# Optimization experiments

Measured on AMD Instinct MI355X. Metric: run time of the kernel, lower is better.

The kernel has to match this reference:

```python
import jax, jax.numpy as jnp
import numpy as np

B, T, D, L, H = 8, 2048, 128, 4, 2
HD = D // H
NITEMS = 200000
EPS = 1e-8  # RMSNorm eps and HSTU denom eps


def _rms(x, s):
    return x * jax.lax.rsqrt(jnp.mean(x * x, axis=-1, keepdims=True) + EPS) * s


def setup_inputs() -> dict:
    key = jax.random.key(0)
    ks = jax.random.split(key, 16)
    g = lambda k, shape: jax.random.normal(k, shape, jnp.float32) * 0.02
    inp = {}
    inp["log_seqs"] = jax.random.randint(ks[0], (B, T), 1, NITEMS + 1)
    inp["attn_mask"] = jnp.tril(jnp.ones((T, T), dtype=bool))  # causal keep-mask
    inp["item_table"] = g(ks[1], (NITEMS + 1, D))
    inp["pos_table"] = g(ks[2], (2 * T + 1, D))
    inp["emb_ln_s"] = jnp.ones((D,), jnp.float32)
    inp["ln1_s"] = jnp.ones((L, D), jnp.float32)
    inp["Uw"] = g(ks[3], (L, D, D)); inp["Ub"] = jnp.zeros((L, D), jnp.float32)
    inp["Vw"] = g(ks[4], (L, D, D)); inp["Vb"] = jnp.zeros((L, D), jnp.float32)
    inp["Qw"] = g(ks[5], (L, D, D)); inp["Qb"] = jnp.zeros((L, D), jnp.float32)
    inp["Kw"] = g(ks[6], (L, D, D)); inp["Kb"] = jnp.zeros((L, D), jnp.float32)
    inp["f2w"] = g(ks[7], (L, D, D)); inp["f2b"] = jnp.zeros((L, D), jnp.float32)
    inp["hstu_ln_s"] = jnp.ones((L, D), jnp.float32)
    inp["ln2_s"] = jnp.ones((L, D), jnp.float32)
    inp["c1w"] = g(ks[8], (L, D, D)); inp["c1b"] = jnp.zeros((L, D), jnp.float32)
    inp["c2w"] = g(ks[9], (L, D, D)); inp["c2b"] = jnp.zeros((L, D), jnp.float32)
    inp["last_ln_s"] = jnp.ones((D,), jnp.float32)
    return inp


def reference(log_seqs, attn_mask, item_table, pos_table, emb_ln_s, ln1_s,
              Uw, Ub, Vw, Vb, Qw, Qb, Kw, Kb, f2w, f2b, hstu_ln_s, ln2_s,
              c1w, c1b, c2w, c2b, last_ln_s):
    positions = jnp.arange(1, T + 1)
    x = item_table[log_seqs] + pos_table[positions][None]  # (B,T,D)
    x = _rms(x, emb_ln_s)
    keep = attn_mask[None, None]  # (1,1,T,T) broadcast over (B,H,T,T)
    scale = 1.0 / np.sqrt(HD)
    for i in range(L):
        q = _rms(x, ln1_s[i])  # pre-norm (norm_first)
        U = jax.nn.silu(q @ Uw[i] + Ub[i])
        V = jax.nn.silu(q @ Vw[i] + Vb[i])
        Q = jax.nn.silu(q @ Qw[i] + Qb[i])
        K = jax.nn.silu(q @ Kw[i] + Kb[i])
        Qh = Q.reshape(B, T, H, HD)
        Kh = K.reshape(B, T, H, HD)
        Vh = V.reshape(B, T, H, HD)
        logits = jnp.einsum('bthd,bshd->bhts', Qh, Kh) * scale  # (B,H,T,T)
        A = jnp.maximum(jax.nn.silu(logits), 0.0)  # SiLU then clamp_min(0)
        A = jnp.where(keep, A, 0.0)
        denom = jnp.sum(A, axis=-1, keepdims=True)
        A = jnp.where(denom > 1e-12, A / (denom + EPS), 0.0)
        AV = jnp.einsum('bhts,bshd->bthd', A, Vh).reshape(B, T, D)
        y = (_rms(AV, hstu_ln_s[i]) * U) @ f2w[i] + f2b[i]
        x = x + y
        f = _rms(x, ln2_s[i])  # pre-norm for FFN
        h = jax.nn.gelu(f @ c1w[i] + c1b[i], approximate=False)  # Conv1d k=1 == Linear
        x = x + (h @ c2w[i] + c2b[i])
    return _rms(x, last_ln_s)
```

## Files before the change

kernel.cpp:

```cpp
#include <hip/hip_runtime.h>
#include <hip/hip_bf16.h>

typedef __bf16 bf16x8 __attribute__((ext_vector_type(8)));
typedef float f32x4 __attribute__((ext_vector_type(4)));
using bf16 = __hip_bfloat16;

constexpr int T = 2048;
constexpr int M = 8 * 2048;

__device__ inline float ldf(const void* p, size_t i, int isf32) {
  if (isf32) return ((const float*)p)[i];
  unsigned u = ((const unsigned short*)p)[i];
  return __uint_as_float(u << 16);
}
__device__ inline float bf2f(unsigned short u) { return __uint_as_float((unsigned)u << 16); }
__device__ inline unsigned short bfb(float x) {
  __hip_bfloat16 h = __float2bfloat16(x);
  return *reinterpret_cast<unsigned short*>(&h);
}

struct PPtrs { const void* p[12]; };

__global__ void detect_convert_k(const void* __restrict__ item, PPtrs ps,
                                 float* __restrict__ params, int* __restrict__ flagp) {
  __shared__ int cnt[4];
  __shared__ int flagLDS;
  int tid = threadIdx.x;
  unsigned short lo = ((const unsigned short*)item)[tid * 2];
  float a = fabsf(bf2f(lo));
  bool okb = (a > 1e-5f) && (a < 0.5f);
  unsigned long long m = __ballot(okb);
  if ((tid & 63) == 0) cnt[tid >> 6] = __popcll(m);
  __syncthreads();
  if (tid == 0) {
    int tot = cnt[0] + cnt[1] + cnt[2] + cnt[3];
    int f = (tot < 128) ? 1 : 0;
    flagLDS = f; *flagp = f;
  }
  __syncthreads();
  int f = flagLDS;
  const int lens[12] = {128, 512, 512, 512, 128, 512, 512, 512, 512, 512, 512, 512};
  int off = 0;
  for (int j = 0; j < 12; ++j) {
    for (int i = tid; i < lens[j]; i += 256) params[off + i] = ldf(ps.p[j], i, f);
    off += lens[j];
  }
}

struct WPtrs { const void* p[7]; };

__global__ void transpose_w_k(WPtrs w, bf16* __restrict__ dst, const int* __restrict__ flagp) {
  int f = *flagp;
  int l = blockIdx.x, wi = blockIdx.y;
  const void* s = w.p[wi];
  size_t sbase = (size_t)l * 16384;
  bf16* d = dst + ((size_t)wi * 4 + l) * 16384;
  for (int i = 0; i < 64; ++i) {
    int e = i * 256 + threadIdx.x;
    d[e] = __float2bfloat16(ldf(s, sbase + (size_t)(e & 127) * 128 + (e >> 7), f));
  }
}

__device__ inline void issueW(const bf16* wt, bf16x8 (&w)[4][8], int quad, int l16) {
  #pragma unroll
  for (int kk = 0; kk < 4; ++kk)
    #pragma unroll
    for (int nt = 0; nt < 8; ++nt)
      w[kk][nt] = *(const bf16x8*)(wt + (size_t)(nt * 16 + l16) * 128 + kk * 32 + quad * 8);
}
__device__ inline void mfma_stage(const bf16x8 (&a)[4], const bf16x8 (&w)[4][8], f32x4 (&acc)[8]) {
  #pragma unroll
  for (int kk = 0; kk < 4; ++kk)
    #pragma unroll
    for (int nt = 0; nt < 8; ++nt)
      acc[nt] = __builtin_amdgcn_mfma_f32_16x16x32_bf16(a[kk], w[kk][nt], acc[nt], 0, 0, 0);
}
__device__ inline void zero8(f32x4 (&acc)[8]) {
  #pragma unroll
  for (int i = 0; i < 8; ++i) acc[i] = (f32x4){0.f, 0.f, 0.f, 0.f};
}
__device__ inline void readA(const bf16* aw, bf16x8 (&a)[4], int quad, int l16) {
  #pragma unroll
  for (int kk = 0; kk < 4; ++kk)
    a[kk] = *(const bf16x8*)&aw[l16 * 136 + kk * 32 + quad * 8];
}
__device__ inline void buildA_rms(const float (&xr)[8][4], const float* scale, bf16* aw,
                                  int quad, int l16) {
  float s8[8];
  #pragma unroll
  for (int nt = 0; nt < 8; ++nt) s8[nt] = scale[nt * 16 + l16];
  #pragma unroll
  for (int r = 0; r < 4; ++r) {
    float ss = 0.f;
    #pragma unroll
    for (int nt = 0; nt < 8; ++nt) ss += xr[nt][r] * xr[nt][r];
    ss += __shfl_xor(ss, 1); ss += __shfl_xor(ss, 2);
    ss += __shfl_xor(ss, 4); ss += __shfl_xor(ss, 8);
    float rs = rsqrtf(ss * (1.f / 128.f) + 1e-8f);
    #pragma unroll
    for (int nt = 0; nt < 8; ++nt)
      aw[(quad * 4 + r) * 136 + nt * 16 + l16] = __float2bfloat16(xr[nt][r] * rs * s8[nt]);
  }
}
__device__ inline void epi_silu_store(const f32x4 (&acc)[8], const float* bias, bf16* outg,
                                      int row0, int quad, int l16, float mulf) {
  #pragma unroll
  for (int nt = 0; nt < 8; ++nt) {
    int col = nt * 16 + l16; float bv = bias[col];
    #pragma unroll
    for (int r = 0; r < 4; ++r) {
      float v = acc[nt][r] + bv;
      v = v / (1.f + __expf(-v)) * mulf;
      outg[(size_t)(row0 + quad * 4 + r) * 128 + col] = __float2bfloat16(v);
    }
  }
}
__device__ inline void epi_silu_vt(const f32x4 (&acc)[8], const float* bias, bf16* vtg,
                                   int row0, int quad, int l16) {
  #pragma unroll
  for (int nt = 0; nt < 8; ++nt) {
    int col = nt * 16 + l16; float bv = bias[col];
    int h = col >> 6, hd = col & 63;
    #pragma unroll
    for (int r = 0; r < 4; ++r) {
      int gr = row0 + quad * 4 + r; int b = gr >> 11, t = gr & 2047;
      float v = acc[nt][r] + bv; v = v / (1.f + __expf(-v));
      vtg[((size_t)(b * 2 + h) * 64 + hd) * 2048 + t] = __float2bfloat16(v);
    }
  }
}
__device__ inline void epi_addx(const f32x4 (&acc)[8], const float* bias, float (&xr)[8][4],
                                int l16) {
  #pragma unroll
  for (int nt = 0; nt < 8; ++nt) {
    float bv = bias[nt * 16 + l16];
    #pragma unroll
    for (int r = 0; r < 4; ++r) xr[nt][r] += acc[nt][r] + bv;
  }
}

__device__ inline void qkvu_stages(const float (&xr)[8][4], bf16* aw, const bf16* wT,
    const float* params, int lnext, bf16* Ug, bf16* Qg, bf16* Kg, bf16* VTg,
    int row0, int quad, int l16) {
  buildA_rms(xr, params + 128 + lnext * 128, aw, quad, l16);
  bf16x8 a[4]; readA(aw, a, quad, l16);
  bf16x8 w[4][8]; f32x4 acc[8];
  const float* pb = params + 1792;
  issueW(wT + (size_t)(0 * 4 + lnext) * 16384, w, quad, l16);
  zero8(acc); mfma_stage(a, w, acc);
  issueW(wT + (size_t)(1 * 4 + lnext) * 16384, w, quad, l16);
  epi_silu_store(acc, pb + 0 * 512 + lnext * 128, Ug, row0, quad, l16, 1.f);
  zero8(acc); mfma_stage(a, w, acc);
  issueW(wT + (size_t)(2 * 4 + lnext) * 16384, w, quad, l16);
  epi_silu_vt(acc, pb + 1 * 512 + lnext * 128, VTg, row0, quad, l16);
  zero8(acc); mfma_stage(a, w, acc);
  issueW(wT + (size_t)(3 * 4 + lnext) * 16384, w, quad, l16);
  epi_silu_store(acc, pb + 2 * 512 + lnext * 128, Qg, row0, quad, l16, 0.125f);
  zero8(acc); mfma_stage(a, w, acc);
  epi_silu_store(acc, pb + 3 * 512 + lnext * 128, Kg, row0, quad, l16, 1.f);
}

__global__ __launch_bounds__(256) void pre_k(const int* __restrict__ seqs,
    const void* __restrict__ item, const void* __restrict__ pos, const bf16* __restrict__ wT,
    const float* __restrict__ params, float* __restrict__ xg, bf16* __restrict__ Ug,
    bf16* __restrict__ Qg, bf16* __restrict__ Kg, bf16* __restrict__ VTg,
    const int* __restrict__ flagp) {
  __shared__ __align__(16) bf16 awAll[4][16 * 136 + 8];
  int f = *flagp;
  int tid = threadIdx.x, wv = tid >> 6, lane = tid & 63, quad = lane >> 4, l16 = lane & 15;
  bf16* aw = awAll[wv];
  int row0 = blockIdx.x * 64 + wv * 16;
  int idxs[4];
  #pragma unroll
  for (int r = 0; r < 4; ++r) idxs[r] = seqs[row0 + quad * 4 + r];
  float xr[8][4];
  #pragma unroll
  for (int nt = 0; nt < 8; ++nt) {
    int col = nt * 16 + l16;
    #pragma unroll
    for (int r = 0; r < 4; ++r) {
      int gr = row0 + quad * 4 + r; int t = gr & 2047;
      xr[nt][r] = ldf(item, (size_t)idxs[r] * 128 + col, f)
                + ldf(pos, (size_t)(t + 1) * 128 + col, f);
    }
  }
  {
    float s8[8];
    #pragma unroll
    for (int nt = 0; nt < 8; ++nt) s8[nt] = params[nt * 16 + l16];
    #pragma unroll
    for (int r = 0; r < 4; ++r) {
      float ss = 0.f;
      #pragma unroll
      for (int nt = 0; nt < 8; ++nt) ss += xr[nt][r] * xr[nt][r];
      ss += __shfl_xor(ss, 1); ss += __shfl_xor(ss, 2);
      ss += __shfl_xor(ss, 4); ss += __shfl_xor(ss, 8);
      float rs = rsqrtf(ss * (1.f / 128.f) + 1e-8f);
      #pragma unroll
      for (int nt = 0; nt < 8; ++nt) xr[nt][r] *= rs * s8[nt];
    }
  }
  #pragma unroll
  for (int nt = 0; nt < 8; ++nt)
    #pragma unroll
    for (int r = 0; r < 4; ++r)
      xg[(size_t)(row0 + quad * 4 + r) * 128 + nt * 16 + l16] = xr[nt][r];
  qkvu_stages(xr, aw, wT, params, 0, Ug, Qg, Kg, VTg, row0, quad, l16);
}

__global__ __launch_bounds__(256) void post_k(int l, float* __restrict__ xg,
    const float* __restrict__ avg, bf16* __restrict__ Ug, bf16* __restrict__ Qg,
    bf16* __restrict__ Kg, bf16* __restrict__ VTg, const bf16* __restrict__ wT,
    const float* __restrict__ params, void* __restrict__ dout, const int* __restrict__ flagp) {
  __shared__ __align__(16) bf16 awAll[4][16 * 136 + 8];
  int tid = threadIdx.x, wv = tid >> 6, lane = tid & 63, quad = lane >> 4, l16 = lane & 15;
  bf16* aw = awAll[wv];
  int row0 = blockIdx.x * 64 + wv * 16;
  bf16x8 w[4][8]; f32x4 acc[8];
  issueW(wT + (size_t)(16 + l) * 16384, w, quad, l16);
  float xr[8][4], av[8][4], uu[8][4];
  #pragma unroll
  for (int nt = 0; nt < 8; ++nt) {
    int col = nt * 16 + l16;
    #pragma unroll
    for (int r = 0; r < 4; ++r) {
      size_t off = (size_t)(row0 + quad * 4 + r) * 128 + col;
      xr[nt][r] = xg[off];
      av[nt][r] = avg[off];
      uu[nt][r] = bf2f(((const unsigned short*)Ug)[off]);
    }
  }
  {
    const float* hs = params + 640 + l * 128;
    float s8[8];
    #pragma unroll
    for (int nt = 0; nt < 8; ++nt) s8[nt] = hs[nt * 16 + l16];
    #pragma unroll
    for (int r = 0; r < 4; ++r) {
      float ss = 0.f;
      #pragma unroll
      for (int nt = 0; nt < 8; ++nt) ss += av[nt][r] * av[nt][r];
      ss += __shfl_xor(ss, 1); ss += __shfl_xor(ss, 2);
      ss += __shfl_xor(ss, 4); ss += __shfl_xor(ss, 8);
      float rs = rsqrtf(ss * (1.f / 128.f) + 1e-8f);
      #pragma unroll
      for (int nt = 0; nt < 8; ++nt)
        aw[(quad * 4 + r) * 136 + nt * 16 + l16] =
            __float2bfloat16(av[nt][r] * rs * s8[nt] * uu[nt][r]);
    }
  }
  bf16x8 a[4]; readA(aw, a, quad, l16);
  zero8(acc); mfma_stage(a, w, acc);
  issueW(wT + (size_t)(20 + l) * 16384, w, quad, l16);
  epi_addx(acc, params + 3840 + l * 128, xr, l16);
  buildA_rms(xr, params + 1152 + l * 128, aw, quad, l16);
  readA(aw, a, quad, l16);
  zero8(acc); mfma_stage(a, w, acc);
  issueW(wT + (size_t)(24 + l) * 16384, w, quad, l16);
  {
    const float* bb = params + 4352 + l * 128;
    #pragma unroll
    for (int nt = 0; nt < 8; ++nt) {
      int col = nt * 16 + l16; float bv = bb[col];
      #pragma unroll
      for (int r = 0; r < 4; ++r) {
        float v = acc[nt][r] + bv;
        v = 0.5f * v * (1.f + erff(v * 0.70710678118f));
        aw[(quad * 4 + r) * 136 + col] = __float2bfloat16(v);
      }
    }
  }
  readA(aw, a, quad, l16);
  zero8(acc); mfma_stage(a, w, acc);
  epi_addx(acc, params + 4864 + l * 128, xr, l16);
  if (l == 3) {
    int f = *flagp;
    const float* ls = params + 1664;
    float s8[8];
    #pragma unroll
    for (int nt = 0; nt < 8; ++nt) s8[nt] = ls[nt * 16 + l16];
    #pragma unroll
    for (int r = 0; r < 4; ++r) {
      float ss = 0.f;
      #pragma unroll
      for (int nt = 0; nt < 8; ++nt) ss += xr[nt][r] * xr[nt][r];
      ss += __shfl_xor(ss, 1); ss += __shfl_xor(ss, 2);
      ss += __shfl_xor(ss, 4); ss += __shfl_xor(ss, 8);
      float rs = rsqrtf(ss * (1.f / 128.f) + 1e-8f);
      #pragma unroll
      for (int nt = 0; nt < 8; ++nt) {
        size_t off = (size_t)(row0 + quad * 4 + r) * 128 + nt * 16 + l16;
        float o = xr[nt][r] * rs * s8[nt];
        if (f) ((float*)dout)[off] = o; else ((unsigned short*)dout)[off] = bfb(o);
      }
    }
    return;
  }
  #pragma unroll
  for (int nt = 0; nt < 8; ++nt)
    #pragma unroll
    for (int r = 0; r < 4; ++r)
      xg[(size_t)(row0 + quad * 4 + r) * 128 + nt * 16 + l16] = xr[nt][r];
  qkvu_stages(xr, aw, wT, params, l + 1, Ug, Qg, Kg, VTg, row0, quad, l16);
}

__device__ inline void fk_loadK(const bf16* kbase, bf16x8 (&kf)[2][4], int quad, int l16) {
  #pragma unroll
  for (int kk = 0; kk < 2; ++kk)
    #pragma unroll
    for (int nt = 0; nt < 4; ++nt)
      kf[kk][nt] = *(const bf16x8*)(kbase + (size_t)(nt * 16 + l16) * 128 + kk * 32 + quad * 8);
}

__device__ inline void flash_body(int kt, int ntile, const bf16* kga, const bf16* vba,
    const bf16x8 (&qf)[2][2], const bf16x8 (&kc)[2][4], bf16x8 (&kn)[2][4],
    f32x4 (&oacc)[2][4], f32x4 (&dacc)[2], const bf16x8& onesf,
    bf16* sm, int r0, int quad, int l16) {
  int s0 = kt * 64;
  bf16x8 vf[2][4];
  #pragma unroll
  for (int kk = 0; kk < 2; ++kk)
    #pragma unroll
    for (int nt = 0; nt < 4; ++nt)
      vf[kk][nt] = *(const bf16x8*)(vba + (size_t)(nt * 16 + l16) * 2048 + s0 + kk * 32 + quad * 8);
  f32x4 sacc[2][4] = {};
  #pragma unroll
  for (int kk = 0; kk < 2; ++kk)
    #pragma unroll
    for (int nt = 0; nt < 4; ++nt) {
      sacc[0][nt] = __builtin_amdgcn_mfma_f32_16x16x32_bf16(qf[0][kk], kc[kk][nt], sacc[0][nt], 0, 0, 0);
      sacc[1][nt] = __builtin_amdgcn_mfma_f32_16x16x32_bf16(qf[1][kk], kc[kk][nt], sacc[1][nt], 0, 0, 0);
    }
  if (kt + 2 < ntile) fk_loadK(kga + (size_t)(s0 + 128) * 128, kn, quad, l16);
  #pragma unroll
  for (int mi = 0; mi < 2; ++mi) {
    int trow = r0 + mi * 16 + quad * 4;
    #pragma unroll
    for (int nt = 0; nt < 4; ++nt) {
      int sc = s0 + nt * 16 + l16;
      #pragma unroll
      for (int r = 0; r < 4; ++r) {
        float v = sacc[mi][nt][r];
        float aa = (sc <= trow + r && v > 0.f) ? v / (1.f + __expf(-v)) : 0.f;
        sm[(mi * 16 + quad * 4 + r) * 72 + nt * 16 + l16] = __float2bfloat16(aa);
      }
    }
  }
  #pragma unroll
  for (int kk = 0; kk < 2; ++kk) {
    bf16x8 af0 = *(const bf16x8*)&sm[l16 * 72 + kk * 32 + quad * 8];
    bf16x8 af1 = *(const bf16x8*)&sm[(16 + l16) * 72 + kk * 32 + quad * 8];
    #pragma unroll
    for (int nt = 0; nt < 4; ++nt) {
      oacc[0][nt] = __builtin_amdgcn_mfma_f32_16x16x32_bf16(af0, vf[kk][nt], oacc[0][nt], 0, 0, 0);
      oacc[1][nt] = __builtin_amdgcn_mfma_f32_16x16x32_bf16(af1, vf[kk][nt], oacc[1][nt], 0, 0, 0);
    }
    dacc[0] = __builtin_amdgcn_mfma_f32_16x16x32_bf16(af0, onesf, dacc[0], 0, 0, 0);
    dacc[1] = __builtin_amdgcn_mfma_f32_16x16x32_bf16(af1, onesf, dacc[1], 0, 0, 0);
  }
}

__global__ __launch_bounds__(128, 2) void flash_k(const bf16* __restrict__ Qg,
    const bf16* __restrict__ Kg, const bf16* __restrict__ VTg, float* __restrict__ avg) {
  __shared__ __align__(16) bf16 smem[2 * 2304];
  int q32 = 63 - (int)blockIdx.x;
  int bh = blockIdx.y, b = bh >> 1, h = bh & 1;
  int tid = threadIdx.x, p = tid >> 6, lane = tid & 63, quad = lane >> 4, l16 = lane & 15;
  int r0 = q32 * 32;
  bf16* sm = smem + p * 2304;
  const bf16* kga = Kg + (size_t)b * 2048 * 128 + h * 64;
  const bf16* vba = VTg + (size_t)bh * 64 * 2048;
  const bf16* qbase = Qg + ((size_t)b * 2048 + r0) * 128 + h * 64;
  bf16x8 qf[2][2];
  #pragma unroll
  for (int mi = 0; mi < 2; ++mi)
    #pragma unroll
    for (int kk = 0; kk < 2; ++kk)
      qf[mi][kk] = *(const bf16x8*)(qbase + (size_t)(mi * 16 + l16) * 128 + kk * 32 + quad * 8);
  bf16x8 onesf;
  #pragma unroll
  for (int j = 0; j < 8; ++j) onesf[j] = (l16 == 0) ? (__bf16)1.0f : (__bf16)0.0f;
  f32x4 oacc[2][4] = {};
  f32x4 dacc[2] = {};
  int ntile = q32 / 2 + 1;
  bf16x8 kA[2][4], kB[2][4];
  int kt = p;
  if (kt < ntile) {
    fk_loadK(kga + (size_t)kt * 64 * 128, kA, quad, l16);
    while (true) {
      flash_body(kt, ntile, kga, vba, qf, kA, kB, oacc, dacc, onesf, sm, r0, quad, l16);
      kt += 2;
      if (kt >= ntile) break;
      flash_body(kt, ntile, kga, vba, qf, kB, kA, oacc, dacc, onesf, sm, r0, quad, l16);
      kt += 2;
      if (kt >= ntile) break;
    }
  }
  __syncthreads();
  float* mo = (float*)smem;
  float* md = mo + 2048;
  if (p == 1) {
    #pragma unroll
    for (int mi = 0; mi < 2; ++mi) {
      #pragma unroll
      for (int nt = 0; nt < 4; ++nt)
        #pragma unroll
        for (int r = 0; r < 4; ++r)
          mo[(mi * 16 + quad * 4 + r) * 64 + nt * 16 + l16] = oacc[mi][nt][r];
      if (l16 == 0) {
        #pragma unroll
        for (int r = 0; r < 4; ++r) md[mi * 16 + quad * 4 + r] = dacc[mi][r];
      }
    }
  }
  __syncthreads();
  if (p == 0) {
    #pragma unroll
    for (int mi = 0; mi < 2; ++mi) {
      #pragma unroll
      for (int r = 0; r < 4; ++r) {
        float dn = __shfl(dacc[mi][r], quad << 4) + md[mi * 16 + quad * 4 + r];
        float inv = (dn > 1e-12f) ? 1.f / (dn + 1e-8f) : 0.f;
        int row = r0 + mi * 16 + quad * 4 + r;
        #pragma unroll
        for (int nt = 0; nt < 4; ++nt) {
          float o = (oacc[mi][nt][r] + mo[(mi * 16 + quad * 4 + r) * 64 + nt * 16 + l16]) * inv;
          avg[((size_t)b * 2048 + row) * 128 + h * 64 + nt * 16 + l16] = o;
        }
      }
    }
  }
}

extern "C" void kernel_launch(void* const* d_in, const int* in_sizes, int n_in,
                              void* d_out, int out_size, void* d_ws, size_t ws_size,
                              hipStream_t stream) {
  const int* seqs = (const int*)d_in[0];
  const void* item = d_in[2];
  const void* pos  = d_in[3];

  float* params = (float*)d_ws;
  int* flagp = (int*)((char*)d_ws + 24 * 1024);
  char* base = (char*)d_ws + 32 * 1024;
  const size_t MB = 1024 * 1024;
  float* x   = (float*)base;
  float* av  = (float*)(base + 8 * MB);
  bf16* Ug   = (bf16*)(base + 16 * MB);
  bf16* Qg   = (bf16*)(base + 20 * MB);
  bf16* Kg   = (bf16*)(base + 24 * MB);
  bf16* VTg  = (bf16*)(base + 28 * MB);
  bf16* wT   = (bf16*)(base + 32 * MB);

  PPtrs pp;
  pp.p[0] = d_in[4];  pp.p[1] = d_in[5];  pp.p[2] = d_in[16]; pp.p[3] = d_in[17];
  pp.p[4] = d_in[22]; pp.p[5] = d_in[7];  pp.p[6] = d_in[9];  pp.p[7] = d_in[11];
  pp.p[8] = d_in[13]; pp.p[9] = d_in[15]; pp.p[10] = d_in[19]; pp.p[11] = d_in[21];
  detect_convert_k<<<1, 256, 0, stream>>>(item, pp, params, flagp);

  WPtrs wp;
  wp.p[0] = d_in[6]; wp.p[1] = d_in[8]; wp.p[2] = d_in[10]; wp.p[3] = d_in[12];
  wp.p[4] = d_in[14]; wp.p[5] = d_in[18]; wp.p[6] = d_in[20];
  transpose_w_k<<<dim3(4, 7), 256, 0, stream>>>(wp, wT, flagp);

  pre_k<<<M / 64, 256, 0, stream>>>(seqs, item, pos, wT, params, x, Ug, Qg, Kg, VTg, flagp);

  for (int l = 0; l < 4; ++l) {
    flash_k<<<dim3(64, 16), 128, 0, stream>>>(Qg, Kg, VTg, av);
    post_k<<<M / 64, 256, 0, stream>>>(l, x, av, Ug, Qg, Kg, VTg, wT, params, d_out, flagp);
  }
}
```

Baseline: 626.3 us.

## Split flash key tiles across four waves with LDS reduction and mask-free interior tiles

The attention kernel now runs four waves per block instead of two, each wave taking every fourth key tile, and K prefetch distance grows to match. Partial outputs and denominators from all four waves go into padded shared memory, and all threads then reduce them cooperatively and write coalesced rows. The causal mask check is skipped on every tile except the diagonal one. This aims to raise parallelism on the short causal rows and trim per-element compare work, at the cost of more shared memory per block and a larger reduction step.

Measured after the change: 1.153 ms. 84.1% more time.

```diff
diff --git a/kernel.cpp b/kernel.cpp
--- a/kernel.cpp
+++ b/kernel.cpp
@@ -331,20 +331,33 @@
       sacc[0][nt] = __builtin_amdgcn_mfma_f32_16x16x32_bf16(qf[0][kk], kc[kk][nt], sacc[0][nt], 0, 0, 0);
       sacc[1][nt] = __builtin_amdgcn_mfma_f32_16x16x32_bf16(qf[1][kk], kc[kk][nt], sacc[1][nt], 0, 0, 0);
     }
-  if (kt + 2 < ntile) fk_loadK(kga + (size_t)(s0 + 128) * 128, kn, quad, l16);
-  #pragma unroll
-  for (int mi = 0; mi < 2; ++mi) {
-    int trow = r0 + mi * 16 + quad * 4;
-    #pragma unroll
-    for (int nt = 0; nt < 4; ++nt) {
-      int sc = s0 + nt * 16 + l16;
-      #pragma unroll
-      for (int r = 0; r < 4; ++r) {
-        float v = sacc[mi][nt][r];
-        float aa = (sc <= trow + r && v > 0.f) ? v / (1.f + __expf(-v)) : 0.f;
-        sm[(mi * 16 + quad * 4 + r) * 72 + nt * 16 + l16] = __float2bfloat16(aa);
+  if (kt + 4 < ntile) fk_loadK(kga + (size_t)(s0 + 256) * 128, kn, quad, l16);
+  if (kt == ntile - 1) {
+    #pragma unroll
+    for (int mi = 0; mi < 2; ++mi) {
+      int trow = r0 + mi * 16 + quad * 4;
+      #pragma unroll
+      for (int nt = 0; nt < 4; ++nt) {
+        int sc = s0 + nt * 16 + l16;
+        #pragma unroll
+        for (int r = 0; r < 4; ++r) {
+          float v = sacc[mi][nt][r];
+          float aa = (sc <= trow + r && v > 0.f) ? v / (1.f + __expf(-v)) : 0.f;
+          sm[(mi * 16 + quad * 4 + r) * 72 + nt * 16 + l16] = __float2bfloat16(aa);
+        }
       }
     }
+  } else {
+    #pragma unroll
+    for (int mi = 0; mi < 2; ++mi)
+      #pragma unroll
+      for (int nt = 0; nt < 4; ++nt)
+        #pragma unroll
+        for (int r = 0; r < 4; ++r) {
+          float v = sacc[mi][nt][r];
+          float aa = (v > 0.f) ? v / (1.f + __expf(-v)) : 0.f;
+          sm[(mi * 16 + quad * 4 + r) * 72 + nt * 16 + l16] = __float2bfloat16(aa);
+        }
   }
   #pragma unroll
   for (int kk = 0; kk < 2; ++kk) {
@@ -360,14 +373,14 @@
   }
 }
 
-__global__ __launch_bounds__(128, 2) void flash_k(const bf16* __restrict__ Qg,
+__global__ __launch_bounds__(256, 4) void flash_k(const bf16* __restrict__ Qg,
     const bf16* __restrict__ Kg, const bf16* __restrict__ VTg, float* __restrict__ avg) {
-  __shared__ __align__(16) bf16 smem[2 * 2304];
+  __shared__ __align__(16) float red[4][2112];
   int q32 = 63 - (int)blockIdx.x;
   int bh = blockIdx.y, b = bh >> 1, h = bh & 1;
-  int tid = threadIdx.x, p = tid >> 6, lane = tid & 63, quad = lane >> 4, l16 = lane & 15;
+  int tid = threadIdx.x, wv = tid >> 6, lane = tid & 63, quad = lane >> 4, l16 = lane & 15;
   int r0 = q32 * 32;
-  bf16* sm = smem + p * 2304;
+  bf16* sm = reinterpret_cast<bf16*>(&red[0][0]) + wv * 2304;
   const bf16* kga = Kg + (size_t)b * 2048 * 128 + h * 64;
   const bf16* vba = VTg + (size_t)bh * 64 * 2048;
   const bf16* qbase = Qg + ((size_t)b * 2048 + r0) * 128 + h * 64;
@@ -384,51 +397,41 @@
   f32x4 dacc[2] = {};
   int ntile = q32 / 2 + 1;
   bf16x8 kA[2][4], kB[2][4];
-  int kt = p;
+  int kt = wv;
   if (kt < ntile) {
     fk_loadK(kga + (size_t)kt * 64 * 128, kA, quad, l16);
     while (true) {
       flash_body(kt, ntile, kga, vba, qf, kA, kB, oacc, dacc, onesf, sm, r0, quad, l16);
-      kt += 2;
+      kt += 4;
       if (kt >= ntile) break;
       flash_body(kt, ntile, kga, vba, qf, kB, kA, oacc, dacc, onesf, sm, r0, quad, l16);
-      kt += 2;
+      kt += 4;
       if (kt >= ntile) break;
     }
   }
   __syncthreads();
-  float* mo = (float*)smem;
-  float* md = mo + 2048;
-  if (p == 1) {
-    #pragma unroll
-    for (int mi = 0; mi < 2; ++mi) {
-      #pragma unroll
-      for (int nt = 0; nt < 4; ++nt)
-        #pragma unroll
-        for (int r = 0; r < 4; ++r)
-          mo[(mi * 16 + quad * 4 + r) * 64 + nt * 16 + l16] = oacc[mi][nt][r];
-      if (l16 == 0) {
-        #pragma unroll
-        for (int r = 0; r < 4; ++r) md[mi * 16 + quad * 4 + r] = dacc[mi][r];
-      }
+  #pragma unroll
+  for (int mi = 0; mi < 2; ++mi) {
+    #pragma unroll
+    for (int nt = 0; nt < 4; ++nt)
+      #pragma unroll
+      for (int r = 0; r < 4; ++r)
+        red[wv][(mi * 16 + quad * 4 + r) * 65 + nt * 16 + l16] = oacc[mi][nt][r];
+    if (l16 == 0) {
+      #pragma unroll
+      for (int r = 0; r < 4; ++r) red[wv][2080 + mi * 16 + quad * 4 + r] = dacc[mi][r];
     }
   }
   __syncthreads();
-  if (p == 0) {
-    #pragma unroll
-    for (int mi = 0; mi < 2; ++mi) {
-      #pragma unroll
-      for (int r = 0; r < 4; ++r) {
-        float dn = __shfl(dacc[mi][r], quad << 4) + md[mi * 16 + quad * 4 + r];
-        float inv = (dn > 1e-12f) ? 1.f / (dn + 1e-8f) : 0.f;
-        int row = r0 + mi * 16 + quad * 4 + r;
-        #pragma unroll
-        for (int nt = 0; nt < 4; ++nt) {
-          float o = (oacc[mi][nt][r] + mo[(mi * 16 + quad * 4 + r) * 64 + nt * 16 + l16]) * inv;
-          avg[((size_t)b * 2048 + row) * 128 + h * 64 + nt * 16 + l16] = o;
-        }
-      }
-    }
+  #pragma unroll
+  for (int j = 0; j < 8; ++j) {
+    int row = wv * 8 + j;
+    float s = red[0][row * 65 + lane] + red[1][row * 65 + lane]
+            + red[2][row * 65 + lane] + red[3][row * 65 + lane];
+    float d = red[0][2080 + row] + red[1][2080 + row]
+            + red[2][2080 + row] + red[3][2080 + row];
+    float inv = (d > 1e-12f) ? 1.f / (d + 1e-8f) : 0.f;
+    avg[((size_t)b * 2048 + r0 + row) * 128 + h * 64 + lane] = s * inv;
   }
 }
 
@@ -465,7 +468,7 @@
   pre_k<<<M / 64, 256, 0, stream>>>(seqs, item, pos, wT, params, x, Ug, Qg, Kg, VTg, flagp);
 
   for (int l = 0; l < 4; ++l) {
-    flash_k<<<dim3(64, 16), 128, 0, stream>>>(Qg, Kg, VTg, av);
+    flash_k<<<dim3(64, 16), 256, 0, stream>>>(Qg, Kg, VTg, av);
     post_k<<<M / 64, 256, 0, stream>>>(l, x, av, Ug, Qg, Kg, VTg, wT, params, d_out, flagp);
   }
 }
```

## Shrink flash query tile to 16 rows and mask only the diagonal tile

Applied to the files above, without the earlier changes.

The flash attention kernel now processes 16 query rows per block instead of 32, doubling the grid and raising launch_bounds occupancy to 4 blocks per SM. The causal mask comparison is applied only on the last (diagonal) key tile; earlier tiles skip the per-element index compare. Smaller tiles give better load balance and more parallelism, but each K/V tile fetched is now reused by half as many query rows, raising K/V memory traffic.

Measured after the change: 1.201 ms. 91.8% more time.

```diff
diff --git a/kernel.cpp b/kernel.cpp
--- a/kernel.cpp
+++ b/kernel.cpp
@@ -313,8 +313,8 @@
 }
 
 __device__ inline void flash_body(int kt, int ntile, const bf16* kga, const bf16* vba,
-    const bf16x8 (&qf)[2][2], const bf16x8 (&kc)[2][4], bf16x8 (&kn)[2][4],
-    f32x4 (&oacc)[2][4], f32x4 (&dacc)[2], const bf16x8& onesf,
+    const bf16x8 (&qf)[2], const bf16x8 (&kc)[2][4], bf16x8 (&kn)[2][4],
+    f32x4 (&oacc)[4], f32x4& dacc, const bf16x8& onesf,
     bf16* sm, int r0, int quad, int l16) {
   int s0 = kt * 64;
   bf16x8 vf[2][4];
@@ -323,66 +323,66 @@
     #pragma unroll
     for (int nt = 0; nt < 4; ++nt)
       vf[kk][nt] = *(const bf16x8*)(vba + (size_t)(nt * 16 + l16) * 2048 + s0 + kk * 32 + quad * 8);
-  f32x4 sacc[2][4] = {};
+  f32x4 sacc[4] = {};
   #pragma unroll
   for (int kk = 0; kk < 2; ++kk)
     #pragma unroll
-    for (int nt = 0; nt < 4; ++nt) {
-      sacc[0][nt] = __builtin_amdgcn_mfma_f32_16x16x32_bf16(qf[0][kk], kc[kk][nt], sacc[0][nt], 0, 0, 0);
-      sacc[1][nt] = __builtin_amdgcn_mfma_f32_16x16x32_bf16(qf[1][kk], kc[kk][nt], sacc[1][nt], 0, 0, 0);
-    }
+    for (int nt = 0; nt < 4; ++nt)
+      sacc[nt] = __builtin_amdgcn_mfma_f32_16x16x32_bf16(qf[kk], kc[kk][nt], sacc[nt], 0, 0, 0);
   if (kt + 2 < ntile) fk_loadK(kga + (size_t)(s0 + 128) * 128, kn, quad, l16);
-  #pragma unroll
-  for (int mi = 0; mi < 2; ++mi) {
-    int trow = r0 + mi * 16 + quad * 4;
+  if (kt == ntile - 1) {
+    int trow = r0 + quad * 4;
     #pragma unroll
     for (int nt = 0; nt < 4; ++nt) {
       int sc = s0 + nt * 16 + l16;
       #pragma unroll
       for (int r = 0; r < 4; ++r) {
-        float v = sacc[mi][nt][r];
+        float v = sacc[nt][r];
         float aa = (sc <= trow + r && v > 0.f) ? v / (1.f + __expf(-v)) : 0.f;
-        sm[(mi * 16 + quad * 4 + r) * 72 + nt * 16 + l16] = __float2bfloat16(aa);
+        sm[(quad * 4 + r) * 72 + nt * 16 + l16] = __float2bfloat16(aa);
       }
     }
+  } else {
+    #pragma unroll
+    for (int nt = 0; nt < 4; ++nt)
+      #pragma unroll
+      for (int r = 0; r < 4; ++r) {
+        float v = sacc[nt][r];
+        float aa = (v > 0.f) ? v / (1.f + __expf(-v)) : 0.f;
+        sm[(quad * 4 + r) * 72 + nt * 16 + l16] = __float2bfloat16(aa);
+      }
   }
   #pragma unroll
   for (int kk = 0; kk < 2; ++kk) {
-    bf16x8 af0 = *(const bf16x8*)&sm[l16 * 72 + kk * 32 + quad * 8];
-    bf16x8 af1 = *(const bf16x8*)&sm[(16 + l16) * 72 + kk * 32 + quad * 8];
-    #pragma unroll
-    for (int nt = 0; nt < 4; ++nt) {
-      oacc[0][nt] = __builtin_amdgcn_mfma_f32_16x16x32_bf16(af0, vf[kk][nt], oacc[0][nt], 0, 0, 0);
-      oacc[1][nt] = __builtin_amdgcn_mfma_f32_16x16x32_bf16(af1, vf[kk][nt], oacc[1][nt], 0, 0, 0);
-    }
-    dacc[0] = __builtin_amdgcn_mfma_f32_16x16x32_bf16(af0, onesf, dacc[0], 0, 0, 0);
-    dacc[1] = __builtin_amdgcn_mfma_f32_16x16x32_bf16(af1, onesf, dacc[1], 0, 0, 0);
-  }
-}
-
-__global__ __launch_bounds__(128, 2) void flash_k(const bf16* __restrict__ Qg,
+    bf16x8 af = *(const bf16x8*)&sm[l16 * 72 + kk * 32 + quad * 8];
+    #pragma unroll
+    for (int nt = 0; nt < 4; ++nt)
+      oacc[nt] = __builtin_amdgcn_mfma_f32_16x16x32_bf16(af, vf[kk][nt], oacc[nt], 0, 0, 0);
+    dacc = __builtin_amdgcn_mfma_f32_16x16x32_bf16(af, onesf, dacc, 0, 0, 0);
+  }
+}
+
+__global__ __launch_bounds__(128, 4) void flash_k(const bf16* __restrict__ Qg,
     const bf16* __restrict__ Kg, const bf16* __restrict__ VTg, float* __restrict__ avg) {
-  __shared__ __align__(16) bf16 smem[2 * 2304];
-  int q32 = 63 - (int)blockIdx.x;
+  __shared__ __align__(16) bf16 smem[2 * 1152];
+  int q16 = 127 - (int)blockIdx.x;
   int bh = blockIdx.y, b = bh >> 1, h = bh & 1;
   int tid = threadIdx.x, p = tid >> 6, lane = tid & 63, quad = lane >> 4, l16 = lane & 15;
-  int r0 = q32 * 32;
-  bf16* sm = smem + p * 2304;
+  int r0 = q16 * 16;
+  bf16* sm = smem + p * 1152;
   const bf16* kga = Kg + (size_t)b * 2048 * 128 + h * 64;
   const bf16* vba = VTg + (size_t)bh * 64 * 2048;
   const bf16* qbase = Qg + ((size_t)b * 2048 + r0) * 128 + h * 64;
-  bf16x8 qf[2][2];
-  #pragma unroll
-  for (int mi = 0; mi < 2; ++mi)
-    #pragma unroll
-    for (int kk = 0; kk < 2; ++kk)
-      qf[mi][kk] = *(const bf16x8*)(qbase + (size_t)(mi * 16 + l16) * 128 + kk * 32 + quad * 8);
+  bf16x8 qf[2];
+  #pragma unroll
+  for (int kk = 0; kk < 2; ++kk)
+    qf[kk] = *(const bf16x8*)(qbase + (size_t)l16 * 128 + kk * 32 + quad * 8);
   bf16x8 onesf;
   #pragma unroll
   for (int j = 0; j < 8; ++j) onesf[j] = (l16 == 0) ? (__bf16)1.0f : (__bf16)0.0f;
-  f32x4 oacc[2][4] = {};
-  f32x4 dacc[2] = {};
-  int ntile = q32 / 2 + 1;
+  f32x4 oacc[4] = {};
+  f32x4 dacc = {0.f, 0.f, 0.f, 0.f};
+  int ntile = q16 / 4 + 1;
   bf16x8 kA[2][4], kB[2][4];
   int kt = p;
   if (kt < ntile) {
@@ -398,35 +398,29 @@
   }
   __syncthreads();
   float* mo = (float*)smem;
-  float* md = mo + 2048;
+  float* md = mo + 1024;
   if (p == 1) {
     #pragma unroll
-    for (int mi = 0; mi < 2; ++mi) {
-      #pragma unroll
-      for (int nt = 0; nt < 4; ++nt)
-        #pragma unroll
-        for (int r = 0; r < 4; ++r)
-          mo[(mi * 16 + quad * 4 + r) * 64 + nt * 16 + l16] = oacc[mi][nt][r];
-      if (l16 == 0) {
-        #pragma unroll
-        for (int r = 0; r < 4; ++r) md[mi * 16 + quad * 4 + r] = dacc[mi][r];
-      }
+    for (int nt = 0; nt < 4; ++nt)
+      #pragma unroll
+      for (int r = 0; r < 4; ++r)
+        mo[(quad * 4 + r) * 64 + nt * 16 + l16] = oacc[nt][r];
+    if (l16 == 0) {
+      #pragma unroll
+      for (int r = 0; r < 4; ++r) md[quad * 4 + r] = dacc[r];
     }
   }
   __syncthreads();
   if (p == 0) {
     #pragma unroll
-    for (int mi = 0; mi < 2; ++mi) {
-      #pragma unroll
-      for (int r = 0; r < 4; ++r) {
-        float dn = __shfl(dacc[mi][r], quad << 4) + md[mi * 16 + quad * 4 + r];
-        float inv = (dn > 1e-12f) ? 1.f / (dn + 1e-8f) : 0.f;
-        int row = r0 + mi * 16 + quad * 4 + r;
-        #pragma unroll
-        for (int nt = 0; nt < 4; ++nt) {
-          float o = (oacc[mi][nt][r] + mo[(mi * 16 + quad * 4 + r) * 64 + nt * 16 + l16]) * inv;
-          avg[((size_t)b * 2048 + row) * 128 + h * 64 + nt * 16 + l16] = o;
-        }
+    for (int r = 0; r < 4; ++r) {
+      float dn = __shfl(dacc[r], quad << 4) + md[quad * 4 + r];
+      float inv = (dn > 1e-12f) ? 1.f / (dn + 1e-8f) : 0.f;
+      int row = r0 + quad * 4 + r;
+      #pragma unroll
+      for (int nt = 0; nt < 4; ++nt) {
+        float o = (oacc[nt][r] + mo[(quad * 4 + r) * 64 + nt * 16 + l16]) * inv;
+        avg[((size_t)b * 2048 + row) * 128 + h * 64 + nt * 16 + l16] = o;
       }
     }
   }
@@ -465,7 +459,7 @@
   pre_k<<<M / 64, 256, 0, stream>>>(seqs, item, pos, wT, params, x, Ug, Qg, Kg, VTg, flagp);
 
   for (int l = 0; l < 4; ++l) {
-    flash_k<<<dim3(64, 16), 128, 0, stream>>>(Qg, Kg, VTg, av);
+    flash_k<<<dim3(128, 16), 128, 0, stream>>>(Qg, Kg, VTg, av);
     post_k<<<M / 64, 256, 0, stream>>>(l, x, av, Ug, Qg, Kg, VTg, wT, params, d_out, flagp);
   }
 }
```
